# Kernel optimization log

Measured on AMD Instinct MI355X. Metric: run time of the kernel, lower is better.

## Reference

```python
import jax, jax.numpy as jnp
import numpy as np

B, T, N = 256, 4096, 64


def setup_inputs() -> dict:
    key = jax.random.key(0)
    u = jax.random.normal(key, (B, T), dtype=jnp.float32)
    # LRU-style stable parameterization: rho chosen so r = exp(-softplus(rho)) = radii
    radii = np.clip(0.9 + 0.0015 * np.arange(N), 1e-6, 1 - 1e-6)
    rho = np.log(np.expm1(-np.log(radii))).astype(np.float32)
    theta = (np.pi * np.arange(N) / N).astype(np.float32)
    return {
        "u": u,
        "rho": jnp.asarray(rho),
        "theta": jnp.asarray(theta),
        "b_real": jnp.ones((N,), jnp.float32),
        "b_imag": jnp.zeros((N,), jnp.float32),
        "c_real": jnp.ones((N,), jnp.float32),
        "c_imag": jnp.zeros((N,), jnp.float32),
    }


def reference(u, rho, theta, b_real, b_imag, c_real, c_imag):
    # lambda = exp(-softplus(rho)) * exp(i*theta), strictly inside unit circle
    r = jnp.exp(-jax.nn.softplus(rho))
    lam = (r.astype(jnp.complex64) * jnp.exp(1j * theta)).astype(jnp.complex64)
    b = (b_real + 1j * b_imag).astype(jnp.complex64)
    c_conj = jnp.conj((c_real + 1j * c_imag).astype(jnp.complex64))
    # precompute driving term b * u_t for all t: (T, B, N)
    bu = jnp.swapaxes(b[None, None, :] * u[:, :, None], 0, 1)

    def step(x, bu_t):
        x = lam * x + bu_t            # (B, N) complex diagonal recurrence
        y_t = jnp.real(x @ c_conj)    # (B,) readout Re(c^H x)
        return x, y_t

    x0 = jnp.zeros((u.shape[0], rho.shape[0]), dtype=jnp.complex64)
    _, ys = jax.lax.scan(step, x0, bu)  # ys: (T, B)
    return jnp.swapaxes(ys, 0, 1)       # (B, T) float32
```

## Files before the change

kernel.cpp:

```cpp
#include <hip/hip_runtime.h>
#include <hip/hip_bf16.h>

#define T_LEN  4096
#define NLAG   5
#define CMAX   ((NLAG - 1) * 128 + 63)
#define ESTR   712
#define ROUNDS ((CMAX + 1) / 64)

typedef __attribute__((ext_vector_type(8))) short short8;
typedef __attribute__((ext_vector_type(4))) float f32x4;

static __device__ __forceinline__ unsigned short f2bf(float f) {
  __hip_bfloat16 h = __float2bfloat16(f);
  return *reinterpret_cast<unsigned short*>(&h);
}

#define CVT8(dst, va, vb) {                                                       \
    short8 _v;                                                                    \
    _v[0] = (short)f2bf((va).x); _v[1] = (short)f2bf((va).y);                     \
    _v[2] = (short)f2bf((va).z); _v[3] = (short)f2bf((va).w);                     \
    _v[4] = (short)f2bf((vb).x); _v[5] = (short)f2bf((vb).y);                     \
    _v[6] = (short)f2bf((vb).z); _v[7] = (short)f2bf((vb).w);                     \
    *reinterpret_cast<short8*>(dst) = _v; }

__global__ __launch_bounds__(512) void ssm_one(
    const float* __restrict__ u, const float* __restrict__ rho,
    const float* __restrict__ theta, const float* __restrict__ br,
    const float* __restrict__ bi, const float* __restrict__ cr,
    const float* __restrict__ ci, float* __restrict__ out) {
  __shared__ __align__(16) unsigned short Ab[2][8192];
  __shared__ __align__(16) unsigned short E8[8 * ESTR];
  __shared__ __align__(16) float pad[8][8][68];

  const int tid = threadIdx.x;
  const int lane = tid & 63;
  const int w = tid >> 6;
  const bool prod = (w >= 4);
  const int pt = tid & 255;

  const int bid = blockIdx.x;
  const int swz = (bid & 7) * 32 + (bid >> 3);
  const int t0 = (swz & 63) * 64;
  const int b0 = (swz >> 6) * 64;

  const int lrow = lane >> 4, lc16 = lane & 15;
  const float4 z4 = make_float4(0.f, 0.f, 0.f, 0.f);
  float4 av[2][4][2];
  f32x4 acc[2][2] = {};

#define ISSUEA(j, S) { _Pragma("unroll") for (int h_ = 0; h_ < 4; ++h_) {         \
    const int hh = pt + 256 * h_;                                                 \
    const int r_ = hh >> 4, cg = hh & 15;                                         \
    const int gg = t0 - (j) * 128 + cg * 8;                                       \
    if ((unsigned)gg < 4096u) {                                                   \
      const float* p_ = u + (size_t)(b0 + r_) * T_LEN + gg;                       \
      av[S][h_][0] = *reinterpret_cast<const float4*>(p_);                        \
      av[S][h_][1] = *reinterpret_cast<const float4*>(p_ + 4);                    \
    } else { av[S][h_][0] = z4; av[S][h_][1] = z4; } } }

#define WRITEA(buf, S) { _Pragma("unroll") for (int h_ = 0; h_ < 4; ++h_) {       \
    const int hh = pt + 256 * h_;                                                 \
    const int r_ = hh >> 4, cg = hh & 15;                                         \
    const int eo = r_ * 128 + ((cg * 8) ^ ((r_ & 7) << 3));                       \
    CVT8(&Ab[buf][eo], av[S][h_][0], av[S][h_][1]); } }

  if (prod) ISSUEA(0, 0);

  {
    const short8 z8 = {};
    for (int c = tid; c < ESTR; c += 512)
      *reinterpret_cast<short8*>(&E8[c * 8]) = z8;
  }

  const float rh = rho[lane], th = theta[lane];
  const float lr2 = -1.4426950408f * log1pf(expf(rh));
  const float rr_ = exp2f(lr2);
  const float lre = rr_ * __cosf(th), lim = rr_ * __sinf(th);
  const float brv = br[lane], biv = bi[lane];
  const float crv = cr[lane], civ = ci[lane];
  const float wre = crv * brv + civ * biv;
  const float wim = crv * biv - civ * brv;

  float Lr[9], Li[9];
  Lr[0] = 1.f; Li[0] = 0.f;
#pragma unroll
  for (int i = 1; i <= 8; ++i) {
    Lr[i] = Lr[i - 1] * lre - Li[i - 1] * lim;
    Li[i] = Lr[i - 1] * lim + Li[i - 1] * lre;
  }

  const float d0f = (float)(8 * ROUNDS * w);
  const float rd0 = exp2f(d0f * lr2);
  float f0 = d0f * (th * 0.15915494309f);
  f0 -= floorf(f0);
  const float a0 = 6.2831853072f * f0;
  const float c0 = __cosf(a0), s0 = __sinf(a0);
  float gr = rd0 * (wre * c0 - wim * s0);
  float gi = rd0 * (wre * s0 + wim * c0);

  __syncthreads();

  {
    float* mypad = &pad[w][0][0];
    const int r2 = lane >> 3, cc = lane & 7;
    for (int rnd = 0; rnd < ROUNDS; ++rnd) {
#pragma unroll
      for (int i2 = 0; i2 < 8; ++i2)
        mypad[i2 * 68 + lane] = gr * Lr[i2] - gi * Li[i2];
      const float ngr = gr * Lr[8] - gi * Li[8];
      const float ngi = gr * Li[8] + gi * Lr[8];
      gr = ngr; gi = ngi;
      const float4 p0 = *reinterpret_cast<const float4*>(&mypad[r2 * 68 + cc * 8]);
      const float4 p1 = *reinterpret_cast<const float4*>(&mypad[r2 * 68 + cc * 8 + 4]);
      float s = ((p0.x + p0.y) + (p0.z + p0.w)) + ((p1.x + p1.y) + (p1.z + p1.w));
      s += __shfl_xor(s, 1); s += __shfl_xor(s, 2); s += __shfl_xor(s, 4);
      const int y = CMAX - (8 * ROUNDS * w + rnd * 8 + r2);
      if (y >= cc) E8[cc * ESTR + (y - cc)] = f2bf(s);
    }
  }

  if (prod) { WRITEA(0, 0); ISSUEA(1, 1); }
  __syncthreads();

#define COMPUTE(jj, buf) {                                                        \
    const unsigned short* A = Ab[buf];                                            \
    const int wm = w >> 1, wn = w & 1;                                            \
    const int pB = 7 - (lc16 & 7);                                                \
    _Pragma("unroll") for (int ks = 0; ks < 4; ++ks) {                            \
      short8 af[2], bfr[2];                                                       \
      _Pragma("unroll") for (int ft = 0; ft < 2; ++ft) {                          \
        const int r = wm * 32 + ft * 16 + lc16;                                   \
        const int pe = (ks * 32 + lrow * 8) ^ ((r & 7) << 3);                     \
        af[ft] = *reinterpret_cast<const short8*>(&A[r * 128 + pe]); }            \
      _Pragma("unroll") for (int fn = 0; fn < 2; ++fn) {                          \
        const int rB = wn * 32 + fn * 16 + lc16;                                  \
        const int x0 = CMAX - (jj) * 128 - rB + ks * 32 + lrow * 8 - pB;          \
        bfr[fn] = *reinterpret_cast<const short8*>(&E8[pB * ESTR + x0]); }        \
      _Pragma("unroll") for (int ft = 0; ft < 2; ++ft)                            \
        _Pragma("unroll") for (int fn = 0; fn < 2; ++fn)                          \
          acc[ft][fn] = __builtin_amdgcn_mfma_f32_16x16x32_bf16(                  \
              af[ft], bfr[fn], acc[ft][fn], 0, 0, 0); } }

#pragma unroll
  for (int j = 0; j < NLAG; ++j) {
    if (prod) {
      if (j + 1 < NLAG) WRITEA((j + 1) & 1, (j + 1) & 1);
      if (j + 2 < NLAG) ISSUEA(j + 2, j & 1);
    } else {
      COMPUTE(j, j & 1);
    }
    if (j < NLAG - 1) __syncthreads();
  }

  if (!prod) {
    const int wm = w >> 1, wn = w & 1;
#pragma unroll
    for (int ft = 0; ft < 2; ++ft)
#pragma unroll
      for (int fn = 0; fn < 2; ++fn)
#pragma unroll
        for (int rg = 0; rg < 4; ++rg) {
          const int row = b0 + wm * 32 + ft * 16 + lrow * 4 + rg;
          const int col = t0 + wn * 32 + fn * 16 + lc16;
          out[(size_t)row * T_LEN + col] = acc[ft][fn][rg];
        }
  }
#undef ISSUEA
#undef WRITEA
#undef COMPUTE
}

extern "C" void kernel_launch(void* const* d_in, const int* in_sizes, int n_in,
                              void* d_out, int out_size, void* d_ws, size_t ws_size,
                              hipStream_t stream) {
  const float* u     = (const float*)d_in[0];
  const float* rho   = (const float*)d_in[1];
  const float* theta = (const float*)d_in[2];
  const float* br    = (const float*)d_in[3];
  const float* bi    = (const float*)d_in[4];
  const float* cr    = (const float*)d_in[5];
  const float* ci    = (const float*)d_in[6];
  float* out = (float*)d_out;

  ssm_one<<<256, 512, 0, stream>>>(u, rho, theta, br, bi, cr, ci, out);
}
```

Measured before the change: 13.26 us.

## Interleave decay-kernel table generation with the lag-pipelined MFMA main loop

The table of bf16 decay coefficients used as the B operand was built entirely in the prologue, with each warp running 9 serial rounds before the main loop started. Round assignment is now strided across warps, and each warp advances by lambda^64, obtained by squaring lambda^8 three times. Only round 0 runs up front; the remaining rounds run two per lag iteration, each just before the barrier that precedes the lag that needs them. The scratch pad is double-buffered so consecutive rounds do not collide. This shortens the serial prologue but lengthens each main-loop step, and the repeated squaring adds small precision drift in the lambda^64 stepping.

```diff
diff --git a/kernel.cpp b/kernel.cpp
--- a/kernel.cpp
+++ b/kernel.cpp
@@ -5,7 +5,7 @@
 #define NLAG   5
 #define CMAX   ((NLAG - 1) * 128 + 63)
 #define ESTR   712
-#define ROUNDS ((CMAX + 1) / 64)
+#define NRND   9
 
 typedef __attribute__((ext_vector_type(8))) short short8;
 typedef __attribute__((ext_vector_type(4))) float f32x4;
@@ -30,7 +30,7 @@
     const float* __restrict__ ci, float* __restrict__ out) {
   __shared__ __align__(16) unsigned short Ab[2][8192];
   __shared__ __align__(16) unsigned short E8[8 * ESTR];
-  __shared__ __align__(16) float pad[8][8][68];
+  __shared__ __align__(16) float pad[2][8][8][68];
 
   const int tid = threadIdx.x;
   const int lane = tid & 63;
@@ -88,8 +88,15 @@
     Lr[i] = Lr[i - 1] * lre - Li[i - 1] * lim;
     Li[i] = Lr[i - 1] * lim + Li[i - 1] * lre;
   }
+  float L64r = Lr[8], L64i = Li[8];
+#pragma unroll
+  for (int q = 0; q < 3; ++q) {
+    const float nr = L64r * L64r - L64i * L64i;
+    const float ni = 2.f * L64r * L64i;
+    L64r = nr; L64i = ni;
+  }
 
-  const float d0f = (float)(8 * ROUNDS * w);
+  const float d0f = (float)(8 * w);
   const float rd0 = exp2f(d0f * lr2);
   float f0 = d0f * (th * 0.15915494309f);
   f0 -= floorf(f0);
@@ -98,27 +105,24 @@
   float gr = rd0 * (wre * c0 - wim * s0);
   float gi = rd0 * (wre * s0 + wim * c0);
 
+  const int r2 = lane >> 3, cc = lane & 7;
+
+#define ROUND(rnd) {                                                              \
+    float* mypad = &pad[(rnd) & 1][w][0][0];                                      \
+    _Pragma("unroll") for (int i2 = 0; i2 < 8; ++i2)                              \
+      mypad[i2 * 68 + lane] = gr * Lr[i2] - gi * Li[i2];        \
+    { const float ngr = gr * L64r - gi * L64i;                                    \
+      const float ngi = gr * L64i + gi * L64r;                                    \
+      gr = ngr; gi = ngi; }                                                       \
+    const float4 p0 = *reinterpret_cast<const float4*>(&mypad[r2 * 68 + cc * 8]); \
+    const float4 p1 = *reinterpret_cast<const float4*>(&mypad[r2 * 68 + cc * 8 + 4]); \
+    float s_ = ((p0.x + p0.y) + (p0.z + p0.w)) + ((p1.x + p1.y) + (p1.z + p1.w)); \
+    s_ += __shfl_xor(s_, 1); s_ += __shfl_xor(s_, 2); s_ += __shfl_xor(s_, 4);    \
+    const int y_ = CMAX - (64 * (rnd) + 8 * w + r2);                              \
+    if (y_ >= cc) E8[cc * ESTR + (y_ - cc)] = f2bf(s_); }
+
   __syncthreads();
-
-  {
-    float* mypad = &pad[w][0][0];
-    const int r2 = lane >> 3, cc = lane & 7;
-    for (int rnd = 0; rnd < ROUNDS; ++rnd) {
-#pragma unroll
-      for (int i2 = 0; i2 < 8; ++i2)
-        mypad[i2 * 68 + lane] = gr * Lr[i2] - gi * Li[i2];
-      const float ngr = gr * Lr[8] - gi * Li[8];
-      const float ngi = gr * Li[8] + gi * Lr[8];
-      gr = ngr; gi = ngi;
-      const float4 p0 = *reinterpret_cast<const float4*>(&mypad[r2 * 68 + cc * 8]);
-      const float4 p1 = *reinterpret_cast<const float4*>(&mypad[r2 * 68 + cc * 8 + 4]);
-      float s = ((p0.x + p0.y) + (p0.z + p0.w)) + ((p1.x + p1.y) + (p1.z + p1.w));
-      s += __shfl_xor(s, 1); s += __shfl_xor(s, 2); s += __shfl_xor(s, 4);
-      const int y = CMAX - (8 * ROUNDS * w + rnd * 8 + r2);
-      if (y >= cc) E8[cc * ESTR + (y - cc)] = f2bf(s);
-    }
-  }
-
+  ROUND(0);
   if (prod) { WRITEA(0, 0); ISSUEA(1, 1); }
   __syncthreads();
 
@@ -149,6 +153,8 @@
     } else {
       COMPUTE(j, j & 1);
     }
+    if (2 * j + 1 < NRND) ROUND(2 * j + 1);
+    if (2 * j + 2 < NRND) ROUND(2 * j + 2);
     if (j < NLAG - 1) __syncthreads();
   }
 
@@ -168,6 +174,7 @@
 #undef ISSUEA
 #undef WRITEA
 #undef COMPUTE
+#undef ROUND
 }
 
 extern "C" void kernel_launch(void* const* d_in, const int* in_sizes, int n_in,
```

Result: no change. 13.36 us (+0.7%).

## Drop producer/consumer split; each wave loads its A fragments directly into registers

Applied to the files above, without the earlier changes.

Removes the producer warp specialization and the LDS staging buffer for the input tile. All eight waves now compute: each wave owns a 16-row by 32-column output slice and loads its own u values from global memory straight into MFMA A-fragment registers, converting to bf16 in registers, with a two-stage register prefetch. This eliminates the per-lag __syncthreads and LDS writes and reads for A and frees LDS, with launch_bounds allowing two blocks per CU. The cost is redundant global loads, since the two waves sharing rows each fetch the same data, and more register pressure from holding the prefetched floats.

```diff
diff --git a/kernel.cpp b/kernel.cpp
--- a/kernel.cpp
+++ b/kernel.cpp
@@ -3,9 +3,9 @@
 
 #define T_LEN  4096
 #define NLAG   5
-#define CMAX   ((NLAG - 1) * 128 + 63)
+#define CMAX   575
 #define ESTR   712
-#define ROUNDS ((CMAX + 1) / 64)
+#define ROUNDS 9
 
 typedef __attribute__((ext_vector_type(8))) short short8;
 typedef __attribute__((ext_vector_type(4))) float f32x4;
@@ -15,28 +15,18 @@
   return *reinterpret_cast<unsigned short*>(&h);
 }
 
-#define CVT8(dst, va, vb) {                                                       \
-    short8 _v;                                                                    \
-    _v[0] = (short)f2bf((va).x); _v[1] = (short)f2bf((va).y);                     \
-    _v[2] = (short)f2bf((va).z); _v[3] = (short)f2bf((va).w);                     \
-    _v[4] = (short)f2bf((vb).x); _v[5] = (short)f2bf((vb).y);                     \
-    _v[6] = (short)f2bf((vb).z); _v[7] = (short)f2bf((vb).w);                     \
-    *reinterpret_cast<short8*>(dst) = _v; }
-
-__global__ __launch_bounds__(512) void ssm_one(
+__global__ __launch_bounds__(512, 2) void ssm_one(
     const float* __restrict__ u, const float* __restrict__ rho,
     const float* __restrict__ theta, const float* __restrict__ br,
     const float* __restrict__ bi, const float* __restrict__ cr,
     const float* __restrict__ ci, float* __restrict__ out) {
-  __shared__ __align__(16) unsigned short Ab[2][8192];
   __shared__ __align__(16) unsigned short E8[8 * ESTR];
   __shared__ __align__(16) float pad[8][8][68];
 
   const int tid = threadIdx.x;
   const int lane = tid & 63;
   const int w = tid >> 6;
-  const bool prod = (w >= 4);
-  const int pt = tid & 255;
+  const int q = w >> 1, h = w & 1;
 
   const int bid = blockIdx.x;
   const int swz = (bid & 7) * 32 + (bid >> 3);
@@ -45,26 +35,31 @@
 
   const int lrow = lane >> 4, lc16 = lane & 15;
   const float4 z4 = make_float4(0.f, 0.f, 0.f, 0.f);
+
+  const float* ubase = u + (size_t)(b0 + q * 16 + lc16) * T_LEN;
+
   float4 av[2][4][2];
-  f32x4 acc[2][2] = {};
+  f32x4 acc[2] = {};
 
-#define ISSUEA(j, S) { _Pragma("unroll") for (int h_ = 0; h_ < 4; ++h_) {         \
-    const int hh = pt + 256 * h_;                                                 \
-    const int r_ = hh >> 4, cg = hh & 15;                                         \
-    const int gg = t0 - (j) * 128 + cg * 8;                                       \
-    if ((unsigned)gg < 4096u) {                                                   \
-      const float* p_ = u + (size_t)(b0 + r_) * T_LEN + gg;                       \
-      av[S][h_][0] = *reinterpret_cast<const float4*>(p_);                        \
-      av[S][h_][1] = *reinterpret_cast<const float4*>(p_ + 4);                    \
-    } else { av[S][h_][0] = z4; av[S][h_][1] = z4; } } }
+#define LOADA(j, S) { _Pragma("unroll") for (int ks_ = 0; ks_ < 4; ++ks_) {       \
+    const int gg = t0 - (j) * 128 + ks_ * 32 + lrow * 8;                          \
+    const bool ok_ = (unsigned)gg < 4096u;        \
+    const float* p_ = ubase + (ok_ ? gg : 0);                                     \
+    float4 v0_ = *reinterpret_cast<const float4*>(p_);                            \
+    float4 v1_ = *reinterpret_cast<const float4*>(p_ + 4);                        \
+    if (!ok_) { v0_ = z4; v1_ = z4; }                                             \
+    av[S][ks_][0] = v0_; av[S][ks_][1] = v1_; } }
 
-#define WRITEA(buf, S) { _Pragma("unroll") for (int h_ = 0; h_ < 4; ++h_) {       \
-    const int hh = pt + 256 * h_;                                                 \
-    const int r_ = hh >> 4, cg = hh & 15;                                         \
-    const int eo = r_ * 128 + ((cg * 8) ^ ((r_ & 7) << 3));                       \
-    CVT8(&Ab[buf][eo], av[S][h_][0], av[S][h_][1]); } }
+#define CVTAF(S) { _Pragma("unroll") for (int ks_ = 0; ks_ < 4; ++ks_) {          \
+    const float4 a_ = av[S][ks_][0], b_ = av[S][ks_][1];                          \
+    short8 v_;                                                                    \
+    v_[0] = (short)f2bf(a_.x); v_[1] = (short)f2bf(a_.y);                         \
+    v_[2] = (short)f2bf(a_.z); v_[3] = (short)f2bf(a_.w);                         \
+    v_[4] = (short)f2bf(b_.x); v_[5] = (short)f2bf(b_.y);                         \
+    v_[6] = (short)f2bf(b_.z); v_[7] = (short)f2bf(b_.w);                         \
+    af[ks_] = v_; } }
 
-  if (prod) ISSUEA(0, 0);
+  LOADA(0, 0);
 
   {
     const short8 z8 = {};
@@ -112,62 +107,48 @@
       gr = ngr; gi = ngi;
       const float4 p0 = *reinterpret_cast<const float4*>(&mypad[r2 * 68 + cc * 8]);
       const float4 p1 = *reinterpret_cast<const float4*>(&mypad[r2 * 68 + cc * 8 + 4]);
-      float s = ((p0.x + p0.y) + (p0.z + p0.w)) + ((p1.x + p1.y) + (p1.z + p1.w));
-      s += __shfl_xor(s, 1); s += __shfl_xor(s, 2); s += __shfl_xor(s, 4);
-      const int y = CMAX - (8 * ROUNDS * w + rnd * 8 + r2);
-      if (y >= cc) E8[cc * ESTR + (y - cc)] = f2bf(s);
+      float s_ = ((p0.x + p0.y) + (p0.z + p0.w)) + ((p1.x + p1.y) + (p1.z + p1.w));
+      s_ += __shfl_xor(s_, 1); s_ += __shfl_xor(s_, 2); s_ += __shfl_xor(s_, 4);
+      const int y_ = CMAX - (8 * ROUNDS * w + rnd * 8 + r2);
+      if (y_ >= cc) E8[cc * ESTR + (y_ - cc)] = f2bf(s_);
     }
   }
 
-  if (prod) { WRITEA(0, 0); ISSUEA(1, 1); }
+  LOADA(1, 1);
   __syncthreads();
 
-#define COMPUTE(jj, buf) {                                                        \
-    const unsigned short* A = Ab[buf];                                            \
-    const int wm = w >> 1, wn = w & 1;                                            \
-    const int pB = 7 - (lc16 & 7);                                                \
-    _Pragma("unroll") for (int ks = 0; ks < 4; ++ks) {                            \
-      short8 af[2], bfr[2];                                                       \
-      _Pragma("unroll") for (int ft = 0; ft < 2; ++ft) {                          \
-        const int r = wm * 32 + ft * 16 + lc16;                                   \
-        const int pe = (ks * 32 + lrow * 8) ^ ((r & 7) << 3);                     \
-        af[ft] = *reinterpret_cast<const short8*>(&A[r * 128 + pe]); }            \
-      _Pragma("unroll") for (int fn = 0; fn < 2; ++fn) {                          \
-        const int rB = wn * 32 + fn * 16 + lc16;                                  \
-        const int x0 = CMAX - (jj) * 128 - rB + ks * 32 + lrow * 8 - pB;          \
-        bfr[fn] = *reinterpret_cast<const short8*>(&E8[pB * ESTR + x0]); }        \
-      _Pragma("unroll") for (int ft = 0; ft < 2; ++ft)                            \
-        _Pragma("unroll") for (int fn = 0; fn < 2; ++fn)                          \
-          acc[ft][fn] = __builtin_amdgcn_mfma_f32_16x16x32_bf16(                  \
-              af[ft], bfr[fn], acc[ft][fn], 0, 0, 0); } }
+  const int pB = 7 - (lc16 & 7);
+#pragma unroll
+  for (int j = 0; j < NLAG; ++j) {
+    short8 af[4];
+    CVTAF(j & 1);
+    if (j + 2 < NLAG) LOADA(j + 2, j & 1);
+#pragma unroll
+    for (int ks = 0; ks < 4; ++ks) {
+      short8 bfr[2];
+#pragma unroll
+      for (int fn = 0; fn < 2; ++fn) {
+        const int rB = h * 32 + fn * 16 + lc16;
+        const int x0 = CMAX - j * 128 - rB + ks * 32 + lrow * 8 - pB;
+        bfr[fn] = *reinterpret_cast<const short8*>(&E8[pB * ESTR + x0]);
+      }
+#pragma unroll
+      for (int fn = 0; fn < 2; ++fn)
+        acc[fn] = __builtin_amdgcn_mfma_f32_16x16x32_bf16(
+            af[ks], bfr[fn], acc[fn], 0, 0, 0);
+    }
+  }
 
 #pragma unroll
-  for (int j = 0; j < NLAG; ++j) {
-    if (prod) {
-      if (j + 1 < NLAG) WRITEA((j + 1) & 1, (j + 1) & 1);
-      if (j + 2 < NLAG) ISSUEA(j + 2, j & 1);
-    } else {
-      COMPUTE(j, j & 1);
+  for (int fn = 0; fn < 2; ++fn)
+#pragma unroll
+    for (int rg = 0; rg < 4; ++rg) {
+      const int row = b0 + q * 16 + lrow * 4 + rg;
+      const int col = t0 + h * 32 + fn * 16 + lc16;
+      out[(size_t)row * T_LEN + col] = acc[fn][rg];
     }
-    if (j < NLAG - 1) __syncthreads();
-  }
-
-  if (!prod) {
-    const int wm = w >> 1, wn = w & 1;
-#pragma unroll
-    for (int ft = 0; ft < 2; ++ft)
-#pragma unroll
-      for (int fn = 0; fn < 2; ++fn)
-#pragma unroll
-        for (int rg = 0; rg < 4; ++rg) {
-          const int row = b0 + wm * 32 + ft * 16 + lrow * 4 + rg;
-          const int col = t0 + wn * 32 + fn * 16 + lc16;
-          out[(size_t)row * T_LEN + col] = acc[ft][fn][rg];
-        }
-  }
-#undef ISSUEA
-#undef WRITEA
-#undef COMPUTE
+#undef LOADA
+#undef CVTAF
 }
 
 extern "C" void kernel_launch(void* const* d_in, const int* in_sizes, int n_in,
```

After: 17.84 us. 34.5% more time.
